# Optimization experiments

Measured on AMD Instinct MI355X. Metric: run time of the kernel, lower is better.

Reference implementation:

```python
import jax, jax.numpy as jnp
import numpy as np

N = 100000      # nodes
E = 1600000     # edges (avg degree 16)
F_IN = 64       # state_size
H = 128         # hidden_channels
L = 3           # nb_hidden_layers


def setup_inputs() -> dict:
    key = jax.random.key(0)
    ks = jax.random.split(key, 10)
    x = jax.random.normal(ks[0], (N, F_IN), dtype=jnp.float32)
    edge_index = jax.random.randint(ks[1], (2, E), 0, N, dtype=jnp.int32)
    # GCNConv params (glorot-ish scale), bias=True by default in PyG
    W1 = jax.random.normal(ks[2], (F_IN, H), jnp.float32) * (1.0 / np.sqrt(F_IN))
    b1 = jnp.zeros((H,), jnp.float32)
    W2 = jax.random.normal(ks[3], (L, H, H), jnp.float32) * (1.0 / np.sqrt(H))
    b2 = jnp.zeros((L, H), jnp.float32)
    W3 = jax.random.normal(ks[4], (H, 1), jnp.float32) * (1.0 / np.sqrt(H))
    b3 = jnp.zeros((1,), jnp.float32)
    return {"x": x, "edge_index": edge_index, "W1": W1, "b1": b1,
            "W2": W2, "b2": b2, "W3": W3, "b3": b3}


def _gcn_norm(edge_index):
    """Add self-loops and compute symmetric normalization (PyG GCNConv default)."""
    loop = jnp.arange(N, dtype=edge_index.dtype)
    src = jnp.concatenate([edge_index[0], loop])  # [E+N]
    dst = jnp.concatenate([edge_index[1], loop])
    deg = jax.ops.segment_sum(jnp.ones_like(dst, dtype=jnp.float32), dst, num_segments=N)
    dinv = jnp.where(deg > 0, jax.lax.rsqrt(deg), 0.0)
    norm = dinv[src] * dinv[dst]                  # [E+N]
    return src, dst, norm


def _gcn_conv(x, src, dst, norm, W, b):
    h = x @ W                                     # [N, F_out] linear first
    msg = h[src] * norm[:, None]                  # gather + scale, [E+N, F_out]
    agg = jax.ops.segment_sum(msg, dst, num_segments=N)  # scatter-add
    return agg + b


def reference(x, edge_index, W1, b1, W2, b2, W3, b3):
    src, dst, norm = _gcn_norm(edge_index)
    h = jax.nn.relu(_gcn_conv(x, src, dst, norm, W1, b1))
    for i in range(L):  # fixed small layer count
        h = jax.nn.relu(_gcn_conv(h, src, dst, norm, W2[i], b2[i]))
    out = _gcn_conv(h, src, dst, norm, W3, b3)    # [N, 1]
    return out
```

## Files before the change

### kernel.cpp

```cpp
#include <hip/hip_runtime.h>
#include <hip/hip_bf16.h>

#define DIV_UP(a,b) (((a)+(b)-1)/(b))

typedef __attribute__((ext_vector_type(8))) short short8v;
typedef __attribute__((ext_vector_type(4))) float f32x4;
typedef _Float16 half8v __attribute__((ext_vector_type(8)));

__device__ inline unsigned short f2bf(float f){
  unsigned u = __float_as_uint(f);
  u += 0x7FFFu + ((u >> 16) & 1u);
  return (unsigned short)(u >> 16);
}
__device__ inline float bf2f(unsigned short h){ return __uint_as_float(((unsigned)h) << 16); }

__global__ __launch_bounds__(256) void k_count_r(const int* __restrict__ dst, int* __restrict__ counts8,
                                                 int E, int N){
  const int g   = blockIdx.x & 7;
  const int bi  = blockIdx.x >> 3;
  const int bpg = gridDim.x >> 3;
  const int chunkE = (E + 7) >> 3;
  const int lo = g*chunkE;
  const int hi = min(lo + chunkE, E);
  int* base = counts8 + (size_t)g*N;
  for (int e = lo + bi*256 + threadIdx.x; e < hi; e += bpg*256)
    atomicAdd(&base[dst[e]], 1);
}

__global__ __launch_bounds__(256) void k_fill_g(const int* __restrict__ src, const int* __restrict__ dst,
                                                const int* __restrict__ rowptr, int* __restrict__ fill,
                                                int* __restrict__ csr, int E, int N){
  const int g   = blockIdx.x & 7;
  const int bi  = blockIdx.x >> 3;
  const int bpg = gridDim.x >> 3;
  const int chunk = (N + 7) >> 3;
  const int lo = g*chunk;
  const int hi = min(lo + chunk, N);
  for (int e = bi*256 + threadIdx.x; e < E; e += bpg*256){
    int d = dst[e];
    if (d >= lo && d < hi){
      int pos = rowptr[d] + atomicAdd(&fill[d], 1);
      csr[pos] = src[e];
    }
  }
}

__global__ __launch_bounds__(1024) void k_scan1(const int* __restrict__ counts8, int* __restrict__ rowptr,
                                                int* __restrict__ bsum, float* __restrict__ dinv, int N){
  __shared__ int s[1024];
  int t = threadIdx.x, g = blockIdx.x*1024 + t;
  int v = 0;
  if (g < N){
    #pragma unroll
    for (int j = 0; j < 8; ++j) v += counts8[(size_t)j*N + g];
    dinv[g] = rsqrtf((float)(v + 1));
  }
  s[t] = v; __syncthreads();
  for (int off = 1; off < 1024; off <<= 1){
    int u = (t >= off) ? s[t-off] : 0; __syncthreads();
    s[t] += u; __syncthreads();
  }
  if (g < N) rowptr[g] = s[t] - v;
  if (t == 1023) bsum[blockIdx.x] = s[1023];
}

__global__ __launch_bounds__(128) void k_scan2(const int* __restrict__ bsum, int* __restrict__ boff,
                                               int nb, int* __restrict__ rowptr, int N){
  __shared__ int s[128];
  int t = threadIdx.x;
  int v = (t < nb) ? bsum[t] : 0;
  s[t] = v; __syncthreads();
  for (int off = 1; off < 128; off <<= 1){
    int u = (t >= off) ? s[t-off] : 0; __syncthreads();
    s[t] += u; __syncthreads();
  }
  if (t < nb) boff[t] = s[t] - v;
  if (t == 127) rowptr[N] = s[127];
}

__global__ __launch_bounds__(1024) void k_scan3(int* __restrict__ rowptr, const int* __restrict__ boff, int N){
  int g = blockIdx.x*1024 + threadIdx.x;
  if (g < N) rowptr[g] += boff[blockIdx.x];
}

__global__ __launch_bounds__(256) void k_split_w(const float* __restrict__ W1, const float* __restrict__ W2,
                                                 unsigned short* __restrict__ W1h, unsigned short* __restrict__ W1l,
                                                 unsigned short* __restrict__ W2h, unsigned short* __restrict__ W2l,
                                                 int L){
  int idx = blockIdx.x*256 + threadIdx.x;
  int n1 = 64*128;
  if (idx < n1){
    int j = idx & 7, lane = (idx >> 3) & 63, t = idx >> 9;
    int kc = t >> 3, nt = t & 7;
    int tcol = lane & 15, quad = lane >> 4;
    int k = kc*32 + quad*8 + j, n = nt*16 + tcol;
    float v = W1[k*128 + n];
    unsigned short hi = f2bf(v);
    W1h[idx] = hi; W1l[idx] = f2bf(v - bf2f(hi));
  } else {
    int idx2 = idx - n1;
    if (idx2 >= L*128*128) return;
    int i = idx2 >> 14, r = idx2 & 16383;
    int j = r & 7, lane = (r >> 3) & 63, t = r >> 9;
    int kc = t >> 3, nt = t & 7;
    int tcol = lane & 15, quad = lane >> 4;
    int k = kc*32 + quad*8 + j, n = nt*16 + tcol;
    float v = W2[(size_t)i*16384 + k*128 + n];
    unsigned short hi = f2bf(v);
    W2h[idx2] = hi; W2l[idx2] = f2bf(v - bf2f(hi));
  }
}

__global__ __launch_bounds__(256) void k_layer1(const float* __restrict__ x, const int* __restrict__ rowptr,
                                                const int* __restrict__ csr, const float* __restrict__ dinv,
                                                const unsigned short* __restrict__ W1h, const unsigned short* __restrict__ W1l,
                                                const float* __restrict__ b1,
                                                const unsigned short* __restrict__ W2h0, const unsigned short* __restrict__ W2l0,
                                                _Float16* __restrict__ pout, int N){
  constexpr int XS = 72, HS = 136;
  __shared__ __align__(16) char smem[32*HS*2*2];
  unsigned short (*Xh)[XS] = (unsigned short(*)[XS])smem;
  unsigned short (*Xl)[XS] = (unsigned short(*)[XS])(smem + 32*XS*2);
  unsigned short (*Hh)[HS] = (unsigned short(*)[HS])smem;
  unsigned short (*Hl)[HS] = (unsigned short(*)[HS])(smem + 32*HS*2);

  const int tid = threadIdx.x;
  const int node0 = blockIdx.x*32;

  {
    const int nl = tid >> 4;
    const int c  = (tid & 15) * 4;
    const float* xc = x + c;
    #pragma unroll
    for (int it = 0; it < 2; ++it){
      int ln = it*16 + nl;
      int node = node0 + ln;
      if (node < N){
        const float dn = dinv[node];
        float4 s = *(const float4*)(x + (size_t)node*64 + c);
        float ax = dn*s.x, ay = dn*s.y, az = dn*s.z, aw = dn*s.w;
        int e = rowptr[node], end = rowptr[node+1];
        for (; e + 4 <= end; e += 4){
          int s0 = csr[e], s1 = csr[e+1], s2 = csr[e+2], s3 = csr[e+3];
          float d0 = dinv[s0], d1 = dinv[s1], d2 = dinv[s2], d3 = dinv[s3];
          float4 v0 = *(const float4*)(xc + (size_t)s0*64);
          float4 v1 = *(const float4*)(xc + (size_t)s1*64);
          float4 v2 = *(const float4*)(xc + (size_t)s2*64);
          float4 v3 = *(const float4*)(xc + (size_t)s3*64);
          ax += d0*v0.x + d1*v1.x + d2*v2.x + d3*v3.x;
          ay += d0*v0.y + d1*v1.y + d2*v2.y + d3*v3.y;
          az += d0*v0.z + d1*v1.z + d2*v2.z + d3*v3.z;
          aw += d0*v0.w + d1*v1.w + d2*v2.w + d3*v3.w;
        }
        for (; e < end; ++e){
          int s0 = csr[e];
          float d0 = dinv[s0];
          float4 v = *(const float4*)(xc + (size_t)s0*64);
          ax += d0*v.x; ay += d0*v.y; az += d0*v.z; aw += d0*v.w;
        }
        float o[4] = {dn*ax, dn*ay, dn*az, dn*aw};
        ushort4 hh, hl;
        unsigned short* hp = (unsigned short*)&hh;
        unsigned short* lp = (unsigned short*)&hl;
        #pragma unroll
        for (int j = 0; j < 4; ++j){
          unsigned short hi = f2bf(o[j]);
          hp[j] = hi; lp[j] = f2bf(o[j] - bf2f(hi));
        }
        *(ushort4*)&Xh[ln][c] = hh;
        *(ushort4*)&Xl[ln][c] = hl;
      }
    }
  }
  __syncthreads();

  const int wv = tid >> 6, lane = tid & 63, quad = lane >> 4, tcol = lane & 15;
  const int wrow = (wv >> 1) * 16;
  const int wcol = (wv & 1) * 64;

  f32x4 acc[4];
  #pragma unroll
  for (int t = 0; t < 4; ++t){ acc[t][0]=0.f; acc[t][1]=0.f; acc[t][2]=0.f; acc[t][3]=0.f; }
  #pragma unroll
  for (int kc = 0; kc < 2; ++kc){
    short8v a_h = *(const short8v*)&Xh[wrow + tcol][kc*32 + quad*8];
    short8v a_l = *(const short8v*)&Xl[wrow + tcol][kc*32 + quad*8];
    #pragma unroll
    for (int ntl = 0; ntl < 4; ++ntl){
      int nt = (wv & 1)*4 + ntl;
      short8v b_h = *(const short8v*)(W1h + ((size_t)(kc*8 + nt)*64 + lane)*8);
      short8v b_l = *(const short8v*)(W1l + ((size_t)(kc*8 + nt)*64 + lane)*8);
      acc[ntl] = __builtin_amdgcn_mfma_f32_16x16x32_bf16(a_h, b_h, acc[ntl], 0, 0, 0);
      acc[ntl] = __builtin_amdgcn_mfma_f32_16x16x32_bf16(a_l, b_h, acc[ntl], 0, 0, 0);
      acc[ntl] = __builtin_amdgcn_mfma_f32_16x16x32_bf16(a_h, b_l, acc[ntl], 0, 0, 0);
    }
  }
  __syncthreads();

  #pragma unroll
  for (int reg = 0; reg < 4; ++reg){
    int lrow = wrow + quad*4 + reg;
    #pragma unroll
    for (int ntl = 0; ntl < 4; ++ntl){
      int col = wcol + ntl*16 + tcol;
      float o = fmaxf(acc[ntl][reg] + b1[col], 0.f);
      unsigned short hi = f2bf(o);
      Hh[lrow][col] = hi;
      Hl[lrow][col] = f2bf(o - bf2f(hi));
    }
  }
  __syncthreads();

  #pragma unroll
  for (int t = 0; t < 4; ++t){ acc[t][0]=0.f; acc[t][1]=0.f; acc[t][2]=0.f; acc[t][3]=0.f; }
  #pragma unroll
  for (int kc = 0; kc < 4; ++kc){
    short8v a_h = *(const short8v*)&Hh[wrow + tcol][kc*32 + quad*8];
    short8v a_l = *(const short8v*)&Hl[wrow + tcol][kc*32 + quad*8];
    #pragma unroll
    for (int ntl = 0; ntl < 4; ++ntl){
      int nt = (wv & 1)*4 + ntl;
      short8v b_h = *(const short8v*)(W2h0 + ((size_t)(kc*8 + nt)*64 + lane)*8);
      short8v b_l = *(const short8v*)(W2l0 + ((size_t)(kc*8 + nt)*64 + lane)*8);
      acc[ntl] = __builtin_amdgcn_mfma_f32_16x16x32_bf16(a_h, b_h, acc[ntl], 0, 0, 0);
      acc[ntl] = __builtin_amdgcn_mfma_f32_16x16x32_bf16(a_l, b_h, acc[ntl], 0, 0, 0);
      acc[ntl] = __builtin_amdgcn_mfma_f32_16x16x32_bf16(a_h, b_l, acc[ntl], 0, 0, 0);
    }
  }
  #pragma unroll
  for (int reg = 0; reg < 4; ++reg){
    int grow = node0 + wrow + quad*4 + reg;
    if (grow < N){
      float sc = dinv[grow];
      _Float16* op = pout + (size_t)grow*128 + wcol + tcol;
      #pragma unroll
      for (int ntl = 0; ntl < 4; ++ntl) op[ntl*16] = (_Float16)(acc[ntl][reg] * sc);
    }
  }
}

__global__ __launch_bounds__(256) void k_fuse2(const _Float16* __restrict__ p, const int* __restrict__ rowptr,
                                               const int* __restrict__ csr, const float* __restrict__ dinv,
                                               const float* __restrict__ bias,
                                               const unsigned short* __restrict__ Bh, const unsigned short* __restrict__ Bl,
                                               _Float16* __restrict__ pout, int N){
  constexpr int HS = 136;
  __shared__ __align__(16) char smem[32*HS*2*2];
  unsigned short (*Hh)[HS] = (unsigned short(*)[HS])smem;
  unsigned short (*Hl)[HS] = (unsigned short(*)[HS])(smem + 32*HS*2);

  const int tid = threadIdx.x;
  const int node0 = blockIdx.x*32;

  {
    const int nl = tid >> 4;
    const int c  = (tid & 15) * 8;
    const _Float16* pc = p + c;
    #pragma unroll
    for (int it = 0; it < 2; ++it){
      int ln = it*16 + nl;
      int node = node0 + ln;
      if (node < N){
        int e = rowptr[node], end = rowptr[node+1];
        half8v sv = *(const half8v*)(p + (size_t)node*128 + c);
        float a[8];
        #pragma unroll
        for (int j = 0; j < 8; ++j) a[j] = (float)sv[j];
        for (; e + 4 <= end; e += 4){
          int s0 = csr[e], s1 = csr[e+1], s2 = csr[e+2], s3 = csr[e+3];
          half8v v0 = *(const half8v*)(pc + (size_t)s0*128);
          half8v v1 = *(const half8v*)(pc + (size_t)s1*128);
          half8v v2 = *(const half8v*)(pc + (size_t)s2*128);
          half8v v3 = *(const half8v*)(pc + (size_t)s3*128);
          #pragma unroll
          for (int j = 0; j < 8; ++j)
            a[j] += (float)v0[j] + (float)v1[j] + (float)v2[j] + (float)v3[j];
        }
        for (; e < end; ++e){
          half8v v = *(const half8v*)(pc + (size_t)csr[e]*128);
          #pragma unroll
          for (int j = 0; j < 8; ++j) a[j] += (float)v[j];
        }
        float d = dinv[node];
        short8v hh, hl;
        #pragma unroll
        for (int j = 0; j < 8; ++j){
          float o = fmaxf(d*a[j] + bias[c+j], 0.f);
          unsigned short hi = f2bf(o);
          hh[j] = (short)hi;
          hl[j] = (short)f2bf(o - bf2f(hi));
        }
        *(short8v*)&Hh[ln][c] = hh;
        *(short8v*)&Hl[ln][c] = hl;
      }
    }
  }
  __syncthreads();

  const int wv = tid >> 6, lane = tid & 63, quad = lane >> 4, tcol = lane & 15;
  const int wrow = (wv >> 1) * 16;
  const int wcol = (wv & 1) * 64;
  f32x4 acc[4];
  #pragma unroll
  for (int t = 0; t < 4; ++t){ acc[t][0]=0.f; acc[t][1]=0.f; acc[t][2]=0.f; acc[t][3]=0.f; }
  #pragma unroll
  for (int kc = 0; kc < 4; ++kc){
    short8v a_h = *(const short8v*)&Hh[wrow + tcol][kc*32 + quad*8];
    short8v a_l = *(const short8v*)&Hl[wrow + tcol][kc*32 + quad*8];
    #pragma unroll
    for (int ntl = 0; ntl < 4; ++ntl){
      int nt = (wv & 1)*4 + ntl;
      short8v b_h = *(const short8v*)(Bh + ((size_t)(kc*8 + nt)*64 + lane)*8);
      short8v b_l = *(const short8v*)(Bl + ((size_t)(kc*8 + nt)*64 + lane)*8);
      acc[ntl] = __builtin_amdgcn_mfma_f32_16x16x32_bf16(a_h, b_h, acc[ntl], 0, 0, 0);
      acc[ntl] = __builtin_amdgcn_mfma_f32_16x16x32_bf16(a_l, b_h, acc[ntl], 0, 0, 0);
      acc[ntl] = __builtin_amdgcn_mfma_f32_16x16x32_bf16(a_h, b_l, acc[ntl], 0, 0, 0);
    }
  }
  #pragma unroll
  for (int reg = 0; reg < 4; ++reg){
    int grow = node0 + wrow + quad*4 + reg;
    if (grow < N){
      float sc = dinv[grow];
      _Float16* op = pout + (size_t)grow*128 + wcol + tcol;
      #pragma unroll
      for (int ntl = 0; ntl < 4; ++ntl) op[ntl*16] = (_Float16)(acc[ntl][reg] * sc);
    }
  }
}

__global__ __launch_bounds__(256) void k_agg_last(const _Float16* __restrict__ p, const int* __restrict__ rowptr,
                                                  const int* __restrict__ csr, const float* __restrict__ dinv,
                                                  const float* __restrict__ bias, const float* __restrict__ W3,
                                                  float* __restrict__ p5, int N){
  const int tid = threadIdx.x;
  const int node = blockIdx.x*16 + (tid >> 4);
  if (node >= N) return;
  const int c = (tid & 15) * 8;
  const _Float16* pc = p + c;
  int e = rowptr[node], end = rowptr[node+1];
  half8v sv = *(const half8v*)(p + (size_t)node*128 + c);
  float a[8];
  #pragma unroll
  for (int j = 0; j < 8; ++j) a[j] = (float)sv[j];
  for (; e + 4 <= end; e += 4){
    int s0 = csr[e], s1 = csr[e+1], s2 = csr[e+2], s3 = csr[e+3];
    half8v v0 = *(const half8v*)(pc + (size_t)s0*128);
    half8v v1 = *(const half8v*)(pc + (size_t)s1*128);
    half8v v2 = *(const half8v*)(pc + (size_t)s2*128);
    half8v v3 = *(const half8v*)(pc + (size_t)s3*128);
    #pragma unroll
    for (int j = 0; j < 8; ++j)
      a[j] += (float)v0[j] + (float)v1[j] + (float)v2[j] + (float)v3[j];
  }
  for (; e < end; ++e){
    half8v v = *(const half8v*)(pc + (size_t)csr[e]*128);
    #pragma unroll
    for (int j = 0; j < 8; ++j) a[j] += (float)v[j];
  }
  float d = dinv[node];
  float sdot = 0.f;
  #pragma unroll
  for (int j = 0; j < 8; ++j){
    float o = fmaxf(d*a[j] + bias[c+j], 0.f);
    sdot += o * W3[c+j];
  }
  #pragma unroll
  for (int m = 8; m >= 1; m >>= 1) sdot += __shfl_xor(sdot, m, 16);
  if ((tid & 15) == 0) p5[node] = d * sdot;
}

__global__ __launch_bounds__(256) void k_agg1(const float* __restrict__ p5, const int* __restrict__ rowptr,
                                              const int* __restrict__ csr, const float* __restrict__ dinv,
                                              const float* __restrict__ b3, float* __restrict__ out, int N){
  int n = blockIdx.x*256 + threadIdx.x;
  if (n >= N) return;
  int e = rowptr[n], end = rowptr[n+1];
  float acc = p5[n];
  for (; e + 4 <= end; e += 4)
    acc += p5[csr[e]] + p5[csr[e+1]] + p5[csr[e+2]] + p5[csr[e+3]];
  for (; e < end; ++e) acc += p5[csr[e]];
  out[n] = dinv[n]*acc + b3[0];
}

extern "C" void kernel_launch(void* const* d_in, const int* in_sizes, int n_in,
                              void* d_out, int out_size, void* d_ws, size_t ws_size,
                              hipStream_t stream){
  const float* x  = (const float*)d_in[0];
  const int*   ei = (const int*)  d_in[1];
  const float* W1 = (const float*)d_in[2];
  const float* b1 = (const float*)d_in[3];
  const float* W2 = (const float*)d_in[4];
  const float* b2 = (const float*)d_in[5];
  const float* W3 = (const float*)d_in[6];
  const float* b3 = (const float*)d_in[7];
  float* out = (float*)d_out;

  const int N = in_sizes[0] / 64;
  const int E = in_sizes[1] / 2;
  const int L = in_sizes[4] / (128*128);
  const int* src = ei;
  const int* dst = ei + E;

  char* ws = (char*)d_ws;
  size_t off = 0;
  auto alloc = [&](size_t bytes){ void* p = ws + off; off += (bytes + 255) & ~(size_t)255; return p; };
  size_t c8b  = (((size_t)N*8*4) + 255) & ~(size_t)255;
  size_t cntb = ((size_t)N*4 + 255) & ~(size_t)255;
  int*   counts8 = (int*)alloc(c8b + cntb);
  int*   fillc   = (int*)((char*)counts8 + c8b);
  int*   rowptr = (int*)  alloc((size_t)(N+1)*4);
  int*   bsum   = (int*)  alloc(128*4);
  int*   boff   = (int*)  alloc(128*4);
  float* dinv   = (float*)alloc((size_t)N*4);
  float* p5     = (float*)alloc((size_t)N*4);
  int*   csr    = (int*)  alloc((size_t)E*4);
  _Float16* pA  = (_Float16*)alloc((size_t)N*128*2);
  _Float16* pB  = (_Float16*)alloc((size_t)N*128*2);
  unsigned short* W1h = (unsigned short*)alloc(64*128*2);
  unsigned short* W1l = (unsigned short*)alloc(64*128*2);
  unsigned short* W2h = (unsigned short*)alloc((size_t)L*128*128*2);
  unsigned short* W2l = (unsigned short*)alloc((size_t)L*128*128*2);
  (void)ws_size; (void)n_in; (void)out_size;

  hipMemsetAsync(counts8, 0, c8b + cntb, stream);

  k_count_r<<<1024,256,0,stream>>>(dst, counts8, E, N);
  int nb = DIV_UP(N,1024);
  k_scan1<<<nb,1024,0,stream>>>(counts8, rowptr, bsum, dinv, N);
  k_scan2<<<1,128,0,stream>>>(bsum, boff, nb, rowptr, N);
  k_scan3<<<nb,1024,0,stream>>>(rowptr, boff, N);
  k_fill_g<<<1024,256,0,stream>>>(src, dst, rowptr, fillc, csr, E, N);

  int wtot = 64*128 + L*128*128;
  k_split_w<<<DIV_UP(wtot,256),256,0,stream>>>(W1, W2, W1h, W1l, W2h, W2l, L);

  k_layer1<<<DIV_UP(N,32),256,0,stream>>>(x, rowptr, csr, dinv, W1h, W1l, b1, W2h, W2l, pA, N);
  _Float16* pin = pA; _Float16* pout = pB;
  for (int i = 1; i < L; ++i){
    k_fuse2<<<DIV_UP(N,32),256,0,stream>>>(pin, rowptr, csr, dinv, b2 + (size_t)(i-1)*128,
                                           W2h + (size_t)i*128*128, W2l + (size_t)i*128*128, pout, N);
    _Float16* t = pin; pin = pout; pout = t;
  }
  k_agg_last<<<DIV_UP(N,16),256,0,stream>>>(pin, rowptr, csr, dinv, b2 + (size_t)(L-1)*128, W3, p5, N);

  k_agg1<<<DIV_UP(N,256),256,0,stream>>>(p5, rowptr, csr, dinv, b3, out, N);
}
```

Measured before the change: 513.6 us.

## Reuse per-group counts as fill offsets and gather pre-scaled fp16 input

CSR construction now turns the eight per-group count arrays into exclusive write offsets inside the scan fixup. The fill kernel then reads each edge once per group chunk instead of every block scanning all edges with a range filter, and the separate fill counter array goes away. A new pre-pass stores x pre-multiplied by dinv in fp16. Layer 1 therefore gathers half-size rows with no per-neighbour dinv lookups, at the cost of an extra pass over x and fp16 rounding of the input features.

```diff
diff --git a/kernel.cpp b/kernel.cpp
--- a/kernel.cpp
+++ b/kernel.cpp
@@ -27,24 +27,6 @@
     atomicAdd(&base[dst[e]], 1);
 }
 
-__global__ __launch_bounds__(256) void k_fill_g(const int* __restrict__ src, const int* __restrict__ dst,
-                                                const int* __restrict__ rowptr, int* __restrict__ fill,
-                                                int* __restrict__ csr, int E, int N){
-  const int g   = blockIdx.x & 7;
-  const int bi  = blockIdx.x >> 3;
-  const int bpg = gridDim.x >> 3;
-  const int chunk = (N + 7) >> 3;
-  const int lo = g*chunk;
-  const int hi = min(lo + chunk, N);
-  for (int e = bi*256 + threadIdx.x; e < E; e += bpg*256){
-    int d = dst[e];
-    if (d >= lo && d < hi){
-      int pos = rowptr[d] + atomicAdd(&fill[d], 1);
-      csr[pos] = src[e];
-    }
-  }
-}
-
 __global__ __launch_bounds__(1024) void k_scan1(const int* __restrict__ counts8, int* __restrict__ rowptr,
                                                 int* __restrict__ bsum, float* __restrict__ dinv, int N){
   __shared__ int s[1024];
@@ -78,9 +60,48 @@
   if (t == 127) rowptr[N] = s[127];
 }
 
-__global__ __launch_bounds__(1024) void k_scan3(int* __restrict__ rowptr, const int* __restrict__ boff, int N){
+__global__ __launch_bounds__(1024) void k_scan3(int* __restrict__ rowptr, const int* __restrict__ boff,
+                                                int* __restrict__ counts8, int N){
   int g = blockIdx.x*1024 + threadIdx.x;
-  if (g < N) rowptr[g] += boff[blockIdx.x];
+  if (g < N){
+    int r = rowptr[g] + boff[blockIdx.x];
+    rowptr[g] = r;
+    #pragma unroll
+    for (int j = 0; j < 8; ++j){
+      int c = counts8[(size_t)j*N + g];
+      counts8[(size_t)j*N + g] = r;
+      r += c;
+    }
+  }
+}
+
+__global__ __launch_bounds__(256) void k_fill2(const int* __restrict__ src, const int* __restrict__ dst,
+                                               int* __restrict__ off8, int* __restrict__ csr, int E, int N){
+  const int g   = blockIdx.x & 7;
+  const int bi  = blockIdx.x >> 3;
+  const int bpg = gridDim.x >> 3;
+  const int chunkE = (E + 7) >> 3;
+  const int lo = g*chunkE;
+  const int hi = min(lo + chunkE, E);
+  int* base = off8 + (size_t)g*N;
+  for (int e = lo + bi*256 + threadIdx.x; e < hi; e += bpg*256){
+    int pos = atomicAdd(&base[dst[e]], 1);
+    csr[pos] = src[e];
+  }
+}
+
+__global__ __launch_bounds__(256) void k_prep_x(const float* __restrict__ x, const float* __restrict__ dinv,
+                                                _Float16* __restrict__ xs, int N){
+  int idx = blockIdx.x*256 + threadIdx.x;
+  if (idx >= N*8) return;
+  int row = idx >> 3, c = (idx & 7) * 8;
+  float d = dinv[row];
+  float4 a = *(const float4*)(x + (size_t)row*64 + c);
+  float4 b = *(const float4*)(x + (size_t)row*64 + c + 4);
+  half8v o;
+  o[0]=(_Float16)(d*a.x); o[1]=(_Float16)(d*a.y); o[2]=(_Float16)(d*a.z); o[3]=(_Float16)(d*a.w);
+  o[4]=(_Float16)(d*b.x); o[5]=(_Float16)(d*b.y); o[6]=(_Float16)(d*b.z); o[7]=(_Float16)(d*b.w);
+  *(half8v*)(xs + (size_t)row*64 + c) = o;
 }
 
 __global__ __launch_bounds__(256) void k_split_w(const float* __restrict__ W1, const float* __restrict__ W2,
@@ -111,7 +132,7 @@
   }
 }
 
-__global__ __launch_bounds__(256) void k_layer1(const float* __restrict__ x, const int* __restrict__ rowptr,
+__global__ __launch_bounds__(256) void k_layer1(const _Float16* __restrict__ xs, const int* __restrict__ rowptr,
                                                 const int* __restrict__ csr, const float* __restrict__ dinv,
                                                 const unsigned short* __restrict__ W1h, const unsigned short* __restrict__ W1l,
                                                 const float* __restrict__ b1,
@@ -128,48 +149,48 @@
   const int node0 = blockIdx.x*32;
 
   {
-    const int nl = tid >> 4;
-    const int c  = (tid & 15) * 4;
-    const float* xc = x + c;
-    #pragma unroll
-    for (int it = 0; it < 2; ++it){
-      int ln = it*16 + nl;
-      int node = node0 + ln;
-      if (node < N){
-        const float dn = dinv[node];
-        float4 s = *(const float4*)(x + (size_t)node*64 + c);
-        float ax = dn*s.x, ay = dn*s.y, az = dn*s.z, aw = dn*s.w;
-        int e = rowptr[node], end = rowptr[node+1];
-        for (; e + 4 <= end; e += 4){
-          int s0 = csr[e], s1 = csr[e+1], s2 = csr[e+2], s3 = csr[e+3];
-          float d0 = dinv[s0], d1 = dinv[s1], d2 = dinv[s2], d3 = dinv[s3];
-          float4 v0 = *(const float4*)(xc + (size_t)s0*64);
-          float4 v1 = *(const float4*)(xc + (size_t)s1*64);
-          float4 v2 = *(const float4*)(xc + (size_t)s2*64);
-          float4 v3 = *(const float4*)(xc + (size_t)s3*64);
-          ax += d0*v0.x + d1*v1.x + d2*v2.x + d3*v3.x;
-          ay += d0*v0.y + d1*v1.y + d2*v2.y + d3*v3.y;
-          az += d0*v0.z + d1*v1.z + d2*v2.z + d3*v3.z;
-          aw += d0*v0.w + d1*v1.w + d2*v2.w + d3*v3.w;
-        }
-        for (; e < end; ++e){
-          int s0 = csr[e];
-          float d0 = dinv[s0];
-          float4 v = *(const float4*)(xc + (size_t)s0*64);
-          ax += d0*v.x; ay += d0*v.y; az += d0*v.z; aw += d0*v.w;
-        }
-        float o[4] = {dn*ax, dn*ay, dn*az, dn*aw};
-        ushort4 hh, hl;
-        unsigned short* hp = (unsigned short*)&hh;
-        unsigned short* lp = (unsigned short*)&hl;
+    const int nl = tid >> 3;
+    const int c  = (tid & 7) * 8;
+    const _Float16* xc = xs + c;
+    int node = node0 + nl;
+    if (node < N){
+      const float dn = dinv[node];
+      int e = rowptr[node], end = rowptr[node+1];
+      half8v sv = *(const half8v*)(xs + (size_t)node*64 + c);
+      float a[8];
+      #pragma unroll
+      for (int j = 0; j < 8; ++j) a[j] = (float)sv[j];
+      for (; e + 4 <= end; e += 4){
+        int s0 = csr[e], s1 = csr[e+1], s2 = csr[e+2], s3 = csr[e+3];
+        half8v v0 = *(const half8v*)(xc + (size_t)s0*64);
+        half8v v1 = *(const half8v*)(xc + (size_t)s1*64);
+        half8v v2 = *(const half8v*)(xc + (size_t)s2*64);
+        half8v v3 = *(const half8v*)(xc + (size_t)s3*64);
         #pragma unroll
-        for (int j = 0; j < 4; ++j){
-          unsigned short hi = f2bf(o[j]);
-          hp[j] = hi; lp[j] = f2bf(o[j] - bf2f(hi));
-        }
-        *(ushort4*)&Xh[ln][c] = hh;
-        *(ushort4*)&Xl[ln][c] = hl;
+        for (int j = 0; j < 8; ++j)
+          a[j] += (float)v0[j] + (float)v1[j] + (float)v2[j] + (float)v3[j];
       }
+      for (; e < end; ++e){
+        half8v v = *(const half8v*)(xc + (size_t)csr[e]*64);
+        #pragma unroll
+        for (int j = 0; j < 8; ++j) a[j] += (float)v[j];
+      }
+      ushort4 hh0, hh1, hl0, hl1;
+      unsigned short* hp0 = (unsigned short*)&hh0;
+      unsigned short* hp1 = (unsigned short*)&hh1;
+      unsigned short* lp0 = (unsigned short*)&hl0;
+      unsigned short* lp1 = (unsigned short*)&hl1;
+      #pragma unroll
+      for (int j = 0; j < 8; ++j){
+        float o = dn * a[j];
+        unsigned short hi = f2bf(o);
+        unsigned short lo = f2bf(o - bf2f(hi));
+        if (j < 4){ hp0[j] = hi; lp0[j] = lo; } else { hp1[j-4] = hi; lp1[j-4] = lo; }
+      }
+      *(ushort4*)&Xh[nl][c]   = hh0;
+      *(ushort4*)&Xh[nl][c+4] = hh1;
+      *(ushort4*)&Xl[nl][c]   = hl0;
+      *(ushort4*)&Xl[nl][c+4] = hl1;
     }
   }
   __syncthreads();
@@ -406,15 +427,14 @@
   size_t off = 0;
   auto alloc = [&](size_t bytes){ void* p = ws + off; off += (bytes + 255) & ~(size_t)255; return p; };
   size_t c8b  = (((size_t)N*8*4) + 255) & ~(size_t)255;
-  size_t cntb = ((size_t)N*4 + 255) & ~(size_t)255;
-  int*   counts8 = (int*)alloc(c8b + cntb);
-  int*   fillc   = (int*)((char*)counts8 + c8b);
+  int*   counts8 = (int*)alloc(c8b);
   int*   rowptr = (int*)  alloc((size_t)(N+1)*4);
   int*   bsum   = (int*)  alloc(128*4);
   int*   boff   = (int*)  alloc(128*4);
   float* dinv   = (float*)alloc((size_t)N*4);
   float* p5     = (float*)alloc((size_t)N*4);
   int*   csr    = (int*)  alloc((size_t)E*4);
+  _Float16* xs  = (_Float16*)alloc((size_t)N*64*2);
   _Float16* pA  = (_Float16*)alloc((size_t)N*128*2);
   _Float16* pB  = (_Float16*)alloc((size_t)N*128*2);
   unsigned short* W1h = (unsigned short*)alloc(64*128*2);
@@ -423,19 +443,21 @@
   unsigned short* W2l = (unsigned short*)alloc((size_t)L*128*128*2);
   (void)ws_size; (void)n_in; (void)out_size;
 
-  hipMemsetAsync(counts8, 0, c8b + cntb, stream);
+  hipMemsetAsync(counts8, 0, c8b, stream);
 
   k_count_r<<<1024,256,0,stream>>>(dst, counts8, E, N);
   int nb = DIV_UP(N,1024);
   k_scan1<<<nb,1024,0,stream>>>(counts8, rowptr, bsum, dinv, N);
   k_scan2<<<1,128,0,stream>>>(bsum, boff, nb, rowptr, N);
-  k_scan3<<<nb,1024,0,stream>>>(rowptr, boff, N);
-  k_fill_g<<<1024,256,0,stream>>>(src, dst, rowptr, fillc, csr, E, N);
+  k_scan3<<<nb,1024,0,stream>>>(rowptr, boff, counts8, N);
+  k_fill2<<<1024,256,0,stream>>>(src, dst, counts8, csr, E, N);
+
+  k_prep_x<<<DIV_UP(N*8,256),256,0,stream>>>(x, dinv, xs, N);
 
   int wtot = 64*128 + L*128*128;
   k_split_w<<<DIV_UP(wtot,256),256,0,stream>>>(W1, W2, W1h, W1l, W2h, W2l, L);
 
-  k_layer1<<<DIV_UP(N,32),256,0,stream>>>(x, rowptr, csr, dinv, W1h, W1l, b1, W2h, W2l, pA, N);
+  k_layer1<<<DIV_UP(N,32),256,0,stream>>>(xs, rowptr, csr, dinv, W1h, W1l, b1, W2h, W2l, pA, N);
   _Float16* pin = pA; _Float16* pout = pB;
   for (int i = 1; i < L; ++i){
     k_fuse2<<<DIV_UP(N,32),256,0,stream>>>(pin, rowptr, csr, dinv, b2 + (size_t)(i-1)*128,
```

Measured after the change: 558.9 us. +8.8%, slower.
